# Performance work log

Hardware: AMD Instinct MI355X
Metric: run time of the kernel (lower is better)

## Reference

```python
import jax, jax.numpy as jnp
import numpy as np

C_IN = 128
C_HID = 128


def setup_inputs() -> dict:
    key = jax.random.key(0)
    ks = jax.random.split(key, 10)
    B, I, J = 1, 384, 384
    x = jax.random.normal(ks[0], (B, I, J, C_IN), dtype=jnp.float32)
    mask = jnp.ones((B, I, J), dtype=jnp.float32)
    # LayerNorm params
    ln_gamma = jnp.ones((C_IN,), jnp.float32)
    ln_beta = jnp.zeros((C_IN,), jnp.float32)
    # Projections (stored as [in, out] for x @ W)
    W_a_p = jax.random.normal(ks[1], (C_IN, C_HID), jnp.float32) * 0.02
    b_a_p = jnp.zeros((C_HID,), jnp.float32)
    W_a_g = jax.random.normal(ks[2], (C_IN, C_HID), jnp.float32) * 0.01
    W_b_p = jax.random.normal(ks[3], (C_IN, C_HID), jnp.float32) * 0.02
    b_b_p = jnp.zeros((C_HID,), jnp.float32)
    W_b_g = jax.random.normal(ks[4], (C_IN, C_HID), jnp.float32) * 0.01
    W_z = jax.random.normal(ks[5], (C_HID, C_IN), jnp.float32) * (0.02 / np.sqrt(C_HID))
    b_z = jnp.zeros((C_IN,), jnp.float32)
    return dict(x=x, mask=mask, ln_gamma=ln_gamma, ln_beta=ln_beta,
                W_a_p=W_a_p, b_a_p=b_a_p, W_a_g=W_a_g,
                W_b_p=W_b_p, b_b_p=b_b_p, W_b_g=W_b_g,
                W_z=W_z, b_z=b_z)


def _layer_norm(x, gamma, beta, eps=1e-5):
    mu = jnp.mean(x, axis=-1, keepdims=True)
    var = jnp.mean(jnp.square(x - mu), axis=-1, keepdims=True)
    return (x - mu) * jax.lax.rsqrt(var + eps) * gamma + beta


def reference(x, mask, ln_gamma, ln_beta, W_a_p, b_a_p, W_a_g, W_b_p, b_b_p, W_b_g, W_z, b_z):
    # x: [B, I, J, C_in], mask: [B, I, J]; outgoing triangle multiplication
    xn = _layer_norm(x, ln_gamma, ln_beta)
    m = mask[..., None]
    a = (xn @ W_a_p + b_a_p) * jax.nn.sigmoid(xn @ W_a_g) * m  # [B,I,J,Ch]
    b = (xn @ W_b_p + b_b_p) * jax.nn.sigmoid(xn @ W_b_g) * m  # [B,I,J,Ch]
    # outgoing: sum over k of a[...,i,k,c] * b[...,k,j,c]
    o = jnp.einsum('bikc,bkjc->bijc', a, b)
    o = o @ W_z + b_z
    return x + o
```

## Files before the change

kernel.cpp:

```cpp
#include <hip/hip_runtime.h>

typedef __bf16 bf16;
typedef bf16 bf16x4 __attribute__((ext_vector_type(4)));
typedef bf16 bf16x8 __attribute__((ext_vector_type(8)));
typedef float f32x4 __attribute__((ext_vector_type(4)));
typedef int ivec4 __attribute__((ext_vector_type(4)));

#define PTOT 147456
#define N384 384

static __device__ __forceinline__ f32x4 mfma16(bf16x8 a, bf16x8 b, f32x4 c) {
  return __builtin_amdgcn_mfma_f32_16x16x32_bf16(a, b, c, 0, 0, 0);
}

static __device__ __forceinline__ void gload_lds16(const bf16* g, bf16* lds) {
  __builtin_amdgcn_global_load_lds(
      (const __attribute__((address_space(1))) void*)g,
      (__attribute__((address_space(3))) void*)lds, 16, 0, 0);
}

__global__ __launch_bounds__(256) void k_prep(
    const float* __restrict__ w0, const float* __restrict__ w1,
    const float* __restrict__ w2, const float* __restrict__ w3,
    const float* __restrict__ w4, bf16* __restrict__ wt)
{
  const int m = blockIdx.x >> 3, n = blockIdx.x & 7;
  const float* src = (m == 0) ? w0 : (m == 1) ? w1 : (m == 2) ? w2 : (m == 3) ? w3 : w4;
  const int t = threadIdx.x;
  const int ks = t >> 6, l = t & 63;
  const int ch = n * 16 + (l & 15);
  const int kb = ks * 32 + (l >> 4) * 8;
  bf16 tmp[8] __attribute__((aligned(16)));
  #pragma unroll
  for (int e = 0; e < 8; ++e)
    tmp[e] = (bf16)src[(size_t)(kb + e) * 128 + ch];
  bf16* dst = (m < 4)
      ? wt + (size_t)((n * 16 + m * 4 + ks) * 64 + l) * 8
      : wt + 4 * 16384 + (size_t)((n * 4 + ks) * 64 + l) * 8;
  *(ivec4*)dst = *(const ivec4*)tmp;
}

__global__ __launch_bounds__(256, 5) void k1_ln_proj(
    const float* __restrict__ x, const float* __restrict__ mask,
    const float* __restrict__ gamma, const float* __restrict__ beta,
    const float* __restrict__ bap, const float* __restrict__ bbp,
    const bf16* __restrict__ wt,
    bf16* __restrict__ a_t, bf16* __restrict__ b_t)
{
  __shared__ __align__(16) bf16 xnb[8192];
  __shared__ __align__(16) bf16 wba[8192];

  const int t = threadIdx.x;
  const int l = t & 63;
  const int w = t >> 6;
  const int p0 = blockIdx.x << 6;
  const int fr = l & 15, fq = l >> 4;
  const int pair = w & 1;
  const int prow0 = (w >> 1) * 32;

  const bf16* wsrc = wt + l * 8;
  const int c0 = w * 4;
  #pragma unroll
  for (int j = 0; j < 4; ++j)
    gload_lds16(wsrc + ((c0 + j) << 9), wba + (c0 + j) * 512);

  f32x4 m4r[2];
  m4r[0] = *(const f32x4*)(mask + p0 + prow0 + fq * 4);
  m4r[1] = *(const f32x4*)(mask + p0 + prow0 + 16 + fq * 4);

  const int csub = (t & 7) << 4;
  f32x4 g4[4], bt4[4];
  #pragma unroll
  for (int i = 0; i < 4; ++i) {
    g4[i]  = *(const f32x4*)(gamma + csub + i * 4);
    bt4[i] = *(const f32x4*)(beta  + csub + i * 4);
  }
  #pragma unroll
  for (int it = 0; it < 2; ++it) {
    const int row = (t >> 3) + it * 32;
    f32x4 v[4];
    const float* xb = x + (size_t)(p0 + row) * 128 + csub;
    #pragma unroll
    for (int i = 0; i < 4; ++i) v[i] = *(const f32x4*)(xb + i * 4);

    float s = 0.f, s2 = 0.f;
    #pragma unroll
    for (int i = 0; i < 4; ++i)
      #pragma unroll
      for (int j = 0; j < 4; ++j) { const float f = v[i][j]; s += f; s2 += f * f; }
    #pragma unroll
    for (int m = 1; m < 8; m <<= 1) {
      s  += __shfl_xor(s, m, 64);
      s2 += __shfl_xor(s2, m, 64);
    }
    const float mu = s * (1.f / 128.f);
    const float rs = rsqrtf(s2 * (1.f / 128.f) - mu * mu + 1e-5f);

    bf16x8 xv0, xv1;
    #pragma unroll
    for (int i = 0; i < 4; ++i)
      #pragma unroll
      for (int j = 0; j < 4; ++j) {
        const float f = (v[i][j] - mu) * rs * g4[i][j] + bt4[i][j];
        const int e = i * 4 + j;
        if (e < 8) xv0[e] = (bf16)f; else xv1[e - 8] = (bf16)f;
      }
    const int sw = (row & 7) << 3;
    *(bf16x8*)&xnb[row * 128 + (csub ^ sw)]       = xv0;
    *(bf16x8*)&xnb[row * 128 + ((csub + 8) ^ sw)] = xv1;
  }
  __syncthreads();

  bf16x8 af[2][4];
  #pragma unroll
  for (int mi = 0; mi < 2; ++mi)
    #pragma unroll
    for (int ks = 0; ks < 4; ++ks) {
      const int row = prow0 + mi * 16 + fr;
      af[mi][ks] = *(const bf16x8*)&xnb[row * 128 + ((ks * 32 + fq * 8) ^ ((fr & 7) << 3))];
    }
  __syncthreads();

  const float* bp = pair ? bbp : bap;
  bf16* dst = pair ? b_t : a_t;
  float biasv[8];
  #pragma unroll
  for (int p = 0; p < 8; ++p) biasv[p] = bp[p * 16 + fr];

  #pragma unroll
  for (int p = 0; p < 8; ++p) {
    if (p < 7) {
      bf16* nb = ((p + 1) & 1) ? xnb : wba;
      #pragma unroll
      for (int j = 0; j < 4; ++j)
        gload_lds16(wsrc + (((p + 1) * 16 + c0 + j) << 9), nb + (c0 + j) * 512);
      __builtin_amdgcn_sched_barrier(0);
    }
    const bf16* buf = ((p & 1) ? xnb : wba) + l * 8;
    const bf16* wpl = buf + (pair * 2) * 2048;
    const bf16* wgl = buf + (pair * 2 + 1) * 2048;

    f32x4 aG0 = (f32x4){0.f, 0.f, 0.f, 0.f};
    f32x4 aG1 = (f32x4){0.f, 0.f, 0.f, 0.f};
    #pragma unroll
    for (int ks = 0; ks < 4; ++ks) {
      const bf16x8 bv = *(const bf16x8*)(wgl + ks * 512);
      aG0 = mfma16(af[0][ks], bv, aG0);
      aG1 = mfma16(af[1][ks], bv, aG1);
    }
    f32x4 aP0 = (f32x4){0.f, 0.f, 0.f, 0.f};
    f32x4 aP1 = (f32x4){0.f, 0.f, 0.f, 0.f};
    #pragma unroll
    for (int ks = 0; ks < 4; ++ks) {
      const bf16x8 bv = *(const bf16x8*)(wpl + ks * 512);
      aP0 = mfma16(af[0][ks], bv, aP0);
      aP1 = mfma16(af[1][ks], bv, aP1);
    }
    const int ch = p * 16 + fr;
    const float bias = biasv[p];
    #pragma unroll
    for (int mi = 0; mi < 2; ++mi) {
      const f32x4 aG = mi ? aG1 : aG0;
      const f32x4 aP = mi ? aP1 : aP0;
      const int pb = prow0 + mi * 16 + fq * 4;
      const f32x4 m4 = m4r[mi];
      bf16x4 pk;
      #pragma unroll
      for (int r = 0; r < 4; ++r) {
        const float sg = 1.f / (1.f + __expf(-aG[r]));
        pk[r] = (bf16)((aP[r] + bias) * sg * m4[r]);
      }
      *(bf16x4*)(dst + (size_t)ch * PTOT + p0 + pb) = pk;
    }
    if (p < 7) {
      asm volatile("s_waitcnt vmcnt(2)" ::: "memory");
      __builtin_amdgcn_sched_barrier(0);
      __builtin_amdgcn_s_barrier();
    }
  }
}

__global__ __launch_bounds__(256, 2) void k2_tri(
    const bf16* __restrict__ a_t, const bf16* __restrict__ b_t, bf16* __restrict__ o_t)
{
  __shared__ __align__(16) bf16 As[2][6144];
  __shared__ __align__(16) bf16 Bs[2][6144];
  const int t = threadIdx.x, l = t & 63, w = t >> 6;
  const int fr = l & 15, fq = l >> 4;
  const int bid = blockIdx.x;
  const int xcd = bid & 7, idx = bid >> 3;
  const int c  = xcd * 16 + (idx >> 2);
  const int ti = idx & 3;
  const int i0 = (ti >> 1) * 192, j0 = (ti & 1) * 192;
  const bf16* ap = a_t + (size_t)c * PTOT;
  const bf16* bp = b_t + (size_t)c * PTOT;
  const int wm = (w >> 1) * 96, wn = (w & 1) * 96;
  const int arA = w * 48 + (l >> 2);
  const int kp1 = t >> 4, jb1 = (t & 15) * 8;
  const int kp2 = t >> 3, jb2 = 128 + (t & 7) * 8;
  const bool two = t < 128;

  f32x4 acc[6][6];
  #pragma unroll
  for (int mi = 0; mi < 6; ++mi)
    #pragma unroll
    for (int ni = 0; ni < 6; ++ni) acc[mi][ni] = (f32x4){0.f, 0.f, 0.f, 0.f};

  ivec4 g10, g11, g20, g21;
  #pragma unroll
  for (int jcall = 0; jcall < 3; ++jcall) {
    const int row = arA + jcall * 16;
    const int scol = ((l & 3) ^ ((row >> 3) & 3)) << 3;
    gload_lds16(ap + (size_t)(i0 + row) * N384 + scol, &As[0][w * 1536 + jcall * 512]);
  }
  g10 = *(const ivec4*)(bp + (size_t)(2 * kp1) * N384 + j0 + jb1);
  g11 = *(const ivec4*)(bp + (size_t)(2 * kp1 + 1) * N384 + j0 + jb1);
  if (two) {
    g20 = *(const ivec4*)(bp + (size_t)(2 * kp2) * N384 + j0 + jb2);
    g21 = *(const ivec4*)(bp + (size_t)(2 * kp2 + 1) * N384 + j0 + jb2);
  }
  {
    union { ivec4 v; unsigned short u[8]; } ua, ub;
    ua.v = g10; ub.v = g11;
    #pragma unroll
    for (int e = 0; e < 8; ++e) {
      const int j = jb1 + e;
      const unsigned int pk = (unsigned int)ua.u[e] | ((unsigned int)ub.u[e] << 16);
      *(unsigned int*)&Bs[0][j * 32 + (((kp1 >> 2) ^ ((j >> 3) & 3)) << 3) + ((kp1 & 3) << 1)] = pk;
    }
    if (two) {
      ua.v = g20; ub.v = g21;
      #pragma unroll
      for (int e = 0; e < 8; ++e) {
        const int j = jb2 + e;
        const unsigned int pk = (unsigned int)ua.u[e] | ((unsigned int)ub.u[e] << 16);
        *(unsigned int*)&Bs[0][j * 32 + (((kp2 >> 2) ^ ((j >> 3) & 3)) << 3) + ((kp2 & 3) << 1)] = pk;
      }
    }
  }

  for (int kt = 0; kt < 12; ++kt) {
    __syncthreads();
    const int cur = kt & 1;
    bf16x8 af[6], bfv[6];
    #pragma unroll
    for (int mi = 0; mi < 6; ++mi) {
      const int row = wm + mi * 16 + fr;
      af[mi] = *(const bf16x8*)&As[cur][row * 32 + ((fq ^ ((row >> 3) & 3)) << 3)];
    }
    #pragma unroll
    for (int ni = 0; ni < 6; ++ni) {
      const int j = wn + ni * 16 + fr;
      bfv[ni] = *(const bf16x8*)&Bs[cur][j * 32 + ((fq ^ ((j >> 3) & 3)) << 3)];
    }
    if (kt < 11) {
      const int k0 = (kt + 1) * 32;
      const int nxt = cur ^ 1;
      #pragma unroll
      for (int jcall = 0; jcall < 3; ++jcall) {
        const int row = arA + jcall * 16;
        const int scol = ((l & 3) ^ ((row >> 3) & 3)) << 3;
        gload_lds16(ap + (size_t)(i0 + row) * N384 + k0 + scol,
                    &As[nxt][w * 1536 + jcall * 512]);
      }
      g10 = *(const ivec4*)(bp + (size_t)(k0 + 2 * kp1) * N384 + j0 + jb1);
      g11 = *(const ivec4*)(bp + (size_t)(k0 + 2 * kp1 + 1) * N384 + j0 + jb1);
      if (two) {
        g20 = *(const ivec4*)(bp + (size_t)(k0 + 2 * kp2) * N384 + j0 + jb2);
        g21 = *(const ivec4*)(bp + (size_t)(k0 + 2 * kp2 + 1) * N384 + j0 + jb2);
      }
    }
    #pragma unroll
    for (int mi = 0; mi < 6; ++mi)
      #pragma unroll
      for (int ni = 0; ni < 6; ++ni)
        acc[mi][ni] = mfma16(bfv[ni], af[mi], acc[mi][ni]);
    if (kt < 11) {
      const int nxt = cur ^ 1;
      union { ivec4 v; unsigned short u[8]; } ua, ub;
      ua.v = g10; ub.v = g11;
      #pragma unroll
      for (int e = 0; e < 8; ++e) {
        const int j = jb1 + e;
        const unsigned int pk = (unsigned int)ua.u[e] | ((unsigned int)ub.u[e] << 16);
        *(unsigned int*)&Bs[nxt][j * 32 + (((kp1 >> 2) ^ ((j >> 3) & 3)) << 3) + ((kp1 & 3) << 1)] = pk;
      }
      if (two) {
        ua.v = g20; ub.v = g21;
        #pragma unroll
        for (int e = 0; e < 8; ++e) {
          const int j = jb2 + e;
          const unsigned int pk = (unsigned int)ua.u[e] | ((unsigned int)ub.u[e] << 16);
          *(unsigned int*)&Bs[nxt][j * 32 + (((kp2 >> 2) ^ ((j >> 3) & 3)) << 3) + ((kp2 & 3) << 1)] = pk;
        }
      }
    }
  }

  bf16* op = o_t + (size_t)c * PTOT;
  #pragma unroll
  for (int mi = 0; mi < 6; ++mi) {
    const int irow = i0 + wm + mi * 16 + fr;
    #pragma unroll
    for (int ni = 0; ni < 6; ++ni) {
      const int jcol = j0 + wn + ni * 16 + fq * 4;
      bf16x4 pk;
      #pragma unroll
      for (int r = 0; r < 4; ++r) pk[r] = (bf16)acc[mi][ni][r];
      *(bf16x4*)(op + (size_t)irow * N384 + jcol) = pk;
    }
  }
}

__global__ __launch_bounds__(256) void k3_out(
    const bf16* __restrict__ o_t, const bf16* __restrict__ wtz,
    const float* __restrict__ x, const float* __restrict__ bz,
    float* __restrict__ out)
{
  __shared__ __align__(16) bf16 Ao[64 * 128];
  const int t = threadIdx.x, l = t & 63, w = t >> 6;
  const int fr = l & 15, fq = l >> 4;
  const int p0 = blockIdx.x << 6;
  const int ps = t & 7, cb = t >> 3;

  #pragma unroll
  for (int rep = 0; rep < 2; ++rep) {
    const int cc = cb + 32 * rep;
    ivec4 d0 = *(const ivec4*)(o_t + (size_t)(2 * cc) * PTOT + p0 + ps * 8);
    ivec4 d1 = *(const ivec4*)(o_t + (size_t)(2 * cc + 1) * PTOT + p0 + ps * 8);
    union { ivec4 v; unsigned short u[8]; } ua, ub;
    ua.v = d0; ub.v = d1;
    #pragma unroll
    for (int e = 0; e < 8; ++e) {
      const int p = ps * 8 + e;
      const unsigned int pk = (unsigned int)ua.u[e] | ((unsigned int)ub.u[e] << 16);
      *(unsigned int*)&Ao[p * 128 + (((cc >> 2) ^ (p & 15)) << 3) + ((cc & 3) << 1)] = pk;
    }
  }
  __syncthreads();

  bf16x8 af[4];
  #pragma unroll
  for (int ks = 0; ks < 4; ++ks) {
    const int p = w * 16 + fr;
    af[ks] = *(const bf16x8*)&Ao[p * 128 + (((ks * 4 + fq) ^ fr) << 3)];
  }

  const bf16* wzf = wtz + l * 8;
  f32x4 acc[8];
  #pragma unroll
  for (int n = 0; n < 8; ++n) acc[n] = (f32x4){0.f, 0.f, 0.f, 0.f};
  #pragma unroll
  for (int n = 0; n < 8; ++n)
    #pragma unroll
    for (int ks = 0; ks < 4; ++ks) {
      const bf16x8 bfv = *(const bf16x8*)(wzf + ((n * 4 + ks) << 9));
      acc[n] = mfma16(bfv, af[ks], acc[n]);
    }

  const int pp = p0 + w * 16 + fr;
  #pragma unroll
  for (int n = 0; n < 8; ++n) {
    const int ch = n * 16 + fq * 4;
    const f32x4 b4 = *(const f32x4*)(bz + ch);
    const size_t idx = (size_t)pp * 128 + ch;
    const f32x4 x4 = *(const f32x4*)(x + idx);
    f32x4 o4;
    #pragma unroll
    for (int r = 0; r < 4; ++r) o4[r] = x4[r] + acc[n][r] + b4[r];
    *(f32x4*)(out + idx) = o4;
  }
}

extern "C" void kernel_launch(void* const* d_in, const int* in_sizes, int n_in,
                              void* d_out, int out_size, void* d_ws, size_t ws_size,
                              hipStream_t stream) {
  const float* x     = (const float*)d_in[0];
  const float* mask  = (const float*)d_in[1];
  const float* gamma = (const float*)d_in[2];
  const float* beta  = (const float*)d_in[3];
  const float* Wap   = (const float*)d_in[4];
  const float* bap   = (const float*)d_in[5];
  const float* Wag   = (const float*)d_in[6];
  const float* Wbp   = (const float*)d_in[7];
  const float* bbp   = (const float*)d_in[8];
  const float* Wbg   = (const float*)d_in[9];
  const float* Wz    = (const float*)d_in[10];
  const float* bz    = (const float*)d_in[11];

  char* ws = (char*)d_ws;
  bf16* wt  = (bf16*)ws;
  bf16* a_t = (bf16*)(ws + 163840);
  bf16* b_t = a_t + (size_t)128 * PTOT;
  bf16* o_t = b_t + (size_t)128 * PTOT;
  float* out = (float*)d_out;

  k_prep<<<40, 256, 0, stream>>>(Wap, Wag, Wbp, Wbg, Wz, wt);
  k1_ln_proj<<<2304, 256, 0, stream>>>(x, mask, gamma, beta, bap, bbp, wt, a_t, b_t);
  k2_tri<<<512, 256, 0, stream>>>(a_t, b_t, o_t);
  k3_out<<<2304, 256, 0, stream>>>(o_t, wt + 4 * 16384, x, bz, out);
}
```

Measured before the change: 119.0 us.

## Process 128 positions per block in LN-projection kernel, each wave computing both a and b

The LN+projection kernel now handles 128 rows per block instead of 64, with each wave owning 32 rows and computing both the a and b projections, where before waves were split across the pair. Each weight tile streamed into LDS is therefore reused over twice as many positions, halving total weight traffic and the block count. The LDS buffer is merged into one 32KB array that first holds normalized x and is then reused as the double buffer for weights. The first weight load is no longer overlapped with the LayerNorm phase, and per-wave register and accumulator work doubles, which may reduce occupancy.

```diff
diff --git a/kernel.cpp b/kernel.cpp
--- a/kernel.cpp
+++ b/kernel.cpp
@@ -47,22 +47,14 @@
     const bf16* __restrict__ wt,
     bf16* __restrict__ a_t, bf16* __restrict__ b_t)
 {
-  __shared__ __align__(16) bf16 xnb[8192];
-  __shared__ __align__(16) bf16 wba[8192];
+  __shared__ __align__(16) bf16 xnb[16384];
 
   const int t = threadIdx.x;
   const int l = t & 63;
   const int w = t >> 6;
-  const int p0 = blockIdx.x << 6;
+  const int p0 = blockIdx.x << 7;
   const int fr = l & 15, fq = l >> 4;
-  const int pair = w & 1;
-  const int prow0 = (w >> 1) * 32;
-
-  const bf16* wsrc = wt + l * 8;
-  const int c0 = w * 4;
-  #pragma unroll
-  for (int j = 0; j < 4; ++j)
-    gload_lds16(wsrc + ((c0 + j) << 9), wba + (c0 + j) * 512);
+  const int prow0 = w * 32;
 
   f32x4 m4r[2];
   m4r[0] = *(const f32x4*)(mask + p0 + prow0 + fq * 4);
@@ -76,7 +68,7 @@
     bt4[i] = *(const f32x4*)(beta  + csub + i * 4);
   }
   #pragma unroll
-  for (int it = 0; it < 2; ++it) {
+  for (int it = 0; it < 4; ++it) {
     const int row = (t >> 3) + it * 32;
     f32x4 v[4];
     const float* xb = x + (size_t)(p0 + row) * 128 + csub;
@@ -121,59 +113,69 @@
     }
   __syncthreads();
 
-  const float* bp = pair ? bbp : bap;
-  bf16* dst = pair ? b_t : a_t;
-  float biasv[8];
-  #pragma unroll
-  for (int p = 0; p < 8; ++p) biasv[p] = bp[p * 16 + fr];
+  float biasA[8], biasB[8];
+  #pragma unroll
+  for (int p = 0; p < 8; ++p) { biasA[p] = bap[p * 16 + fr]; biasB[p] = bbp[p * 16 + fr]; }
+
+  const bf16* wsrc = wt + l * 8;
+  const int c0 = w * 4;
+
+  #pragma unroll
+  for (int j = 0; j < 4; ++j)
+    gload_lds16(wsrc + ((c0 + j) << 9), xnb + (c0 + j) * 512);
+  asm volatile("s_waitcnt vmcnt(0)" ::: "memory");
+  __builtin_amdgcn_sched_barrier(0);
+  __syncthreads();
 
   #pragma unroll
   for (int p = 0; p < 8; ++p) {
     if (p < 7) {
-      bf16* nb = ((p + 1) & 1) ? xnb : wba;
+      bf16* nb = xnb + ((p + 1) & 1) * 8192;
       #pragma unroll
       for (int j = 0; j < 4; ++j)
         gload_lds16(wsrc + (((p + 1) * 16 + c0 + j) << 9), nb + (c0 + j) * 512);
       __builtin_amdgcn_sched_barrier(0);
     }
-    const bf16* buf = ((p & 1) ? xnb : wba) + l * 8;
-    const bf16* wpl = buf + (pair * 2) * 2048;
-    const bf16* wgl = buf + (pair * 2 + 1) * 2048;
-
-    f32x4 aG0 = (f32x4){0.f, 0.f, 0.f, 0.f};
-    f32x4 aG1 = (f32x4){0.f, 0.f, 0.f, 0.f};
-    #pragma unroll
-    for (int ks = 0; ks < 4; ++ks) {
-      const bf16x8 bv = *(const bf16x8*)(wgl + ks * 512);
-      aG0 = mfma16(af[0][ks], bv, aG0);
-      aG1 = mfma16(af[1][ks], bv, aG1);
-    }
-    f32x4 aP0 = (f32x4){0.f, 0.f, 0.f, 0.f};
-    f32x4 aP1 = (f32x4){0.f, 0.f, 0.f, 0.f};
-    #pragma unroll
-    for (int ks = 0; ks < 4; ++ks) {
-      const bf16x8 bv = *(const bf16x8*)(wpl + ks * 512);
-      aP0 = mfma16(af[0][ks], bv, aP0);
-      aP1 = mfma16(af[1][ks], bv, aP1);
-    }
-    const int ch = p * 16 + fr;
-    const float bias = biasv[p];
-    #pragma unroll
-    for (int mi = 0; mi < 2; ++mi) {
-      const f32x4 aG = mi ? aG1 : aG0;
-      const f32x4 aP = mi ? aP1 : aP0;
-      const int pb = prow0 + mi * 16 + fq * 4;
-      const f32x4 m4 = m4r[mi];
-      bf16x4 pk;
-      #pragma unroll
-      for (int r = 0; r < 4; ++r) {
-        const float sg = 1.f / (1.f + __expf(-aG[r]));
-        pk[r] = (bf16)((aP[r] + bias) * sg * m4[r]);
-      }
-      *(bf16x4*)(dst + (size_t)ch * PTOT + p0 + pb) = pk;
+    const bf16* buf = xnb + (p & 1) * 8192 + l * 8;
+    #pragma unroll
+    for (int pair = 0; pair < 2; ++pair) {
+      const bf16* wpl = buf + pair * 4096;
+      const bf16* wgl = wpl + 2048;
+      f32x4 aG0 = (f32x4){0.f, 0.f, 0.f, 0.f};
+      f32x4 aG1 = (f32x4){0.f, 0.f, 0.f, 0.f};
+      #pragma unroll
+      for (int ks = 0; ks < 4; ++ks) {
+        const bf16x8 bv = *(const bf16x8*)(wgl + ks * 512);
+        aG0 = mfma16(af[0][ks], bv, aG0);
+        aG1 = mfma16(af[1][ks], bv, aG1);
+      }
+      f32x4 aP0 = (f32x4){0.f, 0.f, 0.f, 0.f};
+      f32x4 aP1 = (f32x4){0.f, 0.f, 0.f, 0.f};
+      #pragma unroll
+      for (int ks = 0; ks < 4; ++ks) {
+        const bf16x8 bv = *(const bf16x8*)(wpl + ks * 512);
+        aP0 = mfma16(af[0][ks], bv, aP0);
+        aP1 = mfma16(af[1][ks], bv, aP1);
+      }
+      const int ch = p * 16 + fr;
+      const float bias = pair ? biasB[p] : biasA[p];
+      bf16* dst = pair ? b_t : a_t;
+      #pragma unroll
+      for (int mi = 0; mi < 2; ++mi) {
+        const f32x4 aG = mi ? aG1 : aG0;
+        const f32x4 aP = mi ? aP1 : aP0;
+        const f32x4 m4 = m4r[mi];
+        bf16x4 pk;
+        #pragma unroll
+        for (int r = 0; r < 4; ++r) {
+          const float sg = 1.f / (1.f + __expf(-aG[r]));
+          pk[r] = (bf16)((aP[r] + bias) * sg * m4[r]);
+        }
+        *(bf16x4*)(dst + (size_t)ch * PTOT + p0 + prow0 + mi * 16 + fq * 4) = pk;
+      }
     }
     if (p < 7) {
-      asm volatile("s_waitcnt vmcnt(2)" ::: "memory");
+      asm volatile("s_waitcnt vmcnt(4)" ::: "memory");
       __builtin_amdgcn_sched_barrier(0);
       __builtin_amdgcn_s_barrier();
     }
@@ -396,7 +398,7 @@
   float* out = (float*)d_out;
 
   k_prep<<<40, 256, 0, stream>>>(Wap, Wag, Wbp, Wbg, Wz, wt);
-  k1_ln_proj<<<2304, 256, 0, stream>>>(x, mask, gamma, beta, bap, bbp, wt, a_t, b_t);
+  k1_ln_proj<<<1152, 256, 0, stream>>>(x, mask, gamma, beta, bap, bbp, wt, a_t, b_t);
   k2_tri<<<512, 256, 0, stream>>>(a_t, b_t, o_t);
   k3_out<<<2304, 256, 0, stream>>>(o_t, wt + 4 * 16384, x, bz, out);
 }
```

After: 126.4 us. +6.3%, slower.
